# Optimization experiments

Hardware: AMD Instinct MI355X
Metric: run time of the kernel (lower is better)

Reference implementation:

```python
import jax, jax.numpy as jnp
import numpy as np

NUM_REC = 22
P = 24            # nodes per graph
G = 8192          # graphs in batch
N = G * P         # 196608 nodes
E = N * 4         # 786432 edges (avg degree 4)
F_NODE = 96       # 74 chem features + 22 receptor one-hot
F_EDGE = 16
EPS = 1e-5
NEG_SLOPE = 0.2   # GATv2 default negative_slope


def gatv2(x, src, dst, edge_attr, Wl, bl, Wr, br, We, att, bo):
    """PyG GATv2Conv (heads=1, add_self_loops=True, fill_value='mean'), eval mode."""
    n = x.shape[0]
    # self loops with edge_attr = mean of incoming edge attrs per target node
    deg = jax.ops.segment_sum(jnp.ones_like(dst, dtype=x.dtype), dst, num_segments=n)
    loop_attr = jax.ops.segment_sum(edge_attr, dst, num_segments=n) / jnp.maximum(deg, 1.0)[:, None]
    loop = jnp.arange(n, dtype=src.dtype)
    s = jnp.concatenate([src, loop])           # [E+N] source
    d = jnp.concatenate([dst, loop])           # [E+N] target
    ea = jnp.concatenate([edge_attr, loop_attr], axis=0)
    xl = x @ Wl + bl                           # source transform [n, C]
    xr = x @ Wr + br                           # target transform [n, C]
    m = xl[s] + xr[d] + ea @ We                # [E+N, C]
    e = jax.nn.leaky_relu(m, NEG_SLOPE) @ att  # [E+N] attention logits
    # segment softmax over target nodes (every node has its self loop -> no empty segment)
    emax = jax.ops.segment_max(e, d, num_segments=n)
    ez = jnp.exp(e - emax[d])
    denom = jax.ops.segment_sum(ez, d, num_segments=n)
    alpha = ez / denom[d]
    return jax.ops.segment_sum(alpha[:, None] * xl[s], d, num_segments=n) + bo


def batchnorm(h, gamma, beta):
    # training-style BN (batch statistics, biased var) as in torch BatchNorm1d forward
    mu = h.mean(0)
    var = h.var(0)
    return gamma * (h - mu) * jax.lax.rsqrt(var + EPS) + beta


def setup_inputs() -> dict:
    key = jax.random.key(0)
    ks = jax.random.split(key, 40)
    x = jax.random.normal(ks[0], (N, F_NODE), jnp.float32)
    # intra-graph, self-loop-free edges
    src = jax.random.randint(ks[1], (E,), 0, N)
    off = jax.random.randint(ks[2], (E,), 1, P)
    dst = (src // P) * P + (src % P + off) % P
    edge_index = jnp.stack([src, dst]).astype(jnp.int32)
    edge_attr = jax.random.normal(ks[3], (E, F_EDGE), jnp.float32)
    batch = (jnp.arange(N) // P).astype(jnp.int32)

    def lin(k, i, o):
        return jax.random.normal(k, (i, o), jnp.float32) * 0.1

    def vec(k, o):
        return jax.random.normal(k, (o,), jnp.float32) * 0.1

    Fin = F_NODE - NUM_REC  # 74
    return {
        "x": x, "edge_index": edge_index, "edge_attr": edge_attr, "batch": batch,
        # GATv2 layer 1 (74 -> 32)
        "Wl1": lin(ks[4], Fin, 32), "bl1": vec(ks[5], 32),
        "Wr1": lin(ks[6], Fin, 32), "br1": vec(ks[7], 32),
        "We1": lin(ks[8], F_EDGE, 32), "att1": vec(ks[9], 32), "bo1": vec(ks[10], 32),
        # GATv2 layer 2 (32 -> 8)
        "Wl2": lin(ks[11], 32, 8), "bl2": vec(ks[12], 8),
        "Wr2": lin(ks[13], 32, 8), "br2": vec(ks[14], 8),
        "We2": lin(ks[15], F_EDGE, 8), "att2": vec(ks[16], 8), "bo2": vec(ks[17], 8),
        # BatchNorm affine
        "g1": jnp.ones((32,), jnp.float32), "be1": jnp.zeros((32,), jnp.float32),
        "g2": jnp.ones((8,), jnp.float32), "be2": jnp.zeros((8,), jnp.float32),
        # MLP head (8+22=30 -> 32 -> 16 -> 8 -> 4 -> 2)
        "fc1_W": lin(ks[18], 8 + NUM_REC, 32), "fc1_b": vec(ks[19], 32),
        "fc2_W": lin(ks[20], 32, 16), "fc2_b": vec(ks[21], 16),
        "fc3_W": lin(ks[22], 16, 8), "fc3_b": vec(ks[23], 8),
        "fc4_W": lin(ks[24], 8, 4), "fc4_b": vec(ks[25], 4),
        "out_W": lin(ks[26], 4, 2), "out_b": vec(ks[27], 2),
    }


def reference(x, edge_index, edge_attr, batch,
              Wl1, bl1, Wr1, br1, We1, att1, bo1,
              Wl2, bl2, Wr2, br2, We2, att2, bo2,
              g1, be1, g2, be2,
              fc1_W, fc1_b, fc2_W, fc2_b, fc3_W, fc3_b, fc4_W, fc4_b, out_W, out_b):
    src, dst = edge_index[0], edge_index[1]
    # per-graph receptor features = last NUM_REC cols of the first node of each graph
    first_idx = jnp.searchsorted(batch, jnp.arange(G, dtype=batch.dtype))
    rec_feat = x[first_idx, -NUM_REC:]                       # [G, 22]
    xin = x[:, :-NUM_REC]                                    # [N, 74]

    h = jax.nn.relu(gatv2(xin, src, dst, edge_attr, Wl1, bl1, Wr1, br1, We1, att1, bo1))
    h = batchnorm(h, g1, be1)                                # [N, 32]
    h = jax.nn.sigmoid(gatv2(h, src, dst, edge_attr, Wl2, bl2, Wr2, br2, We2, att2, bo2))
    h = batchnorm(h, g2, be2)                                # [N, 8]

    cnt = jax.ops.segment_sum(jnp.ones((x.shape[0], 1), x.dtype), batch, num_segments=G)
    pooled = jax.ops.segment_sum(h, batch, num_segments=G) / cnt  # global_mean_pool [G, 8]

    z = jnp.concatenate([pooled, rec_feat], axis=1)          # [G, 30]
    z = jax.nn.relu(z @ fc1_W + fc1_b)
    z = jax.nn.relu(z @ fc2_W + fc2_b)
    z = jax.nn.relu(z @ fc3_W + fc3_b)
    z = jax.nn.relu(z @ fc4_W + fc4_b)
    return z @ out_W + out_b                                 # [G, 2]
```

## Files before the change

kernel.cpp:

```cpp
#include <hip/hip_runtime.h>

typedef unsigned short u16;
typedef unsigned int   u32;
typedef __attribute__((ext_vector_type(4))) float f4_t;
typedef __attribute__((ext_vector_type(4))) unsigned short us4_t;
typedef __attribute__((ext_vector_type(4))) unsigned int   u4_t;

#define GG 8192
#define PP 24
#define NN 196608
#define EE 786432
#define CAP 176

#define oWl1 0
#define oWr1 2368
#define obl1 4736
#define obr1 4768
#define oWe1 4800
#define oatt1 5312
#define obo1 5344
#define oWl2 5376
#define oWr2 5632
#define obl2 5888
#define obr2 5896
#define oWe2 5904
#define oatt2 6032
#define obo2 6040
#define ofc1W 6048
#define ofc1b 7008
#define ofc2W 7040
#define ofc2b 7552
#define ofc3W 7568
#define ofc3b 7696
#define ofc4W 7704
#define ofc4b 7736
#define ooutW 7740
#define ooutb 7748

#define oW1I 0
#define oW2P 4864
#define oB2P 5376

__device__ __forceinline__ float bf2f(u16 u){
  union { u32 i; float f; } x; x.i = ((u32)u) << 16; return x.f;
}
__device__ __forceinline__ u32 fkey(float f){
  int i = __float_as_int(f);
  return (i >= 0) ? (((u32)i) | 0x80000000u) : ~((u32)i);
}
__device__ __forceinline__ float funkey(u32 k){
  u32 i = (k & 0x80000000u) ? (k & 0x7FFFFFFFu) : ~k;
  return __uint_as_float(i);
}
__device__ __forceinline__ float lrelu(float m){ return m > 0.f ? m : 0.2f*m; }
__device__ __forceinline__ float sexp(float a){ return __expf(fminf(a, 0.f)); }
__device__ __forceinline__ float ldf(const void* p, size_t i, int isf){
  return isf ? ((const float*)p)[i] : bf2f(((const u16*)p)[i]);
}

__global__ void k_zero(float* __restrict__ out){
  int i = blockIdx.x*256 + threadIdx.x;
  if(i < GG*2) out[i] = 0.f;
}

__global__ void k_count(const int* __restrict__ dst, int* __restrict__ cnt){
  int e = blockIdx.x*256 + threadIdx.x;
  if(e < EE){
    u32 d = (u32)dst[e];
    if(d < (u32)NN) atomicAdd(&cnt[d], 1);
  }
}

__global__ void k_scanA(const int* __restrict__ cnt, int* __restrict__ offs,
                        int* __restrict__ bsum){
  __shared__ int part[1024];
  int t = threadIdx.x;
  int i = blockIdx.x*1024 + t;
  int c = cnt[i];
  part[t] = c; __syncthreads();
  for(int off=1; off<1024; off<<=1){
    int v = (t>=off) ? part[t-off] : 0;
    __syncthreads();
    part[t] += v;
    __syncthreads();
  }
  offs[i] = part[t] - c;
  if(t==1023) bsum[blockIdx.x] = part[1023];
}

__global__ void k_scanB(int* __restrict__ bsum, int* __restrict__ offs){
  __shared__ int part[256];
  int t = threadIdx.x;
  int c = (t < 192) ? bsum[t] : 0;
  part[t] = c; __syncthreads();
  for(int off=1; off<256; off<<=1){
    int v = (t>=off) ? part[t-off] : 0;
    __syncthreads();
    part[t] += v;
    __syncthreads();
  }
  if(t < 192) bsum[t] = part[t] - c;
  if(t == 255) offs[NN] = part[255];
}

__global__ void k_scanC(int* __restrict__ offs, const int* __restrict__ bsum,
                        int* __restrict__ cursor){
  int t = threadIdx.x;
  int i = blockIdx.x*1024 + t;
  int v = offs[i] + bsum[blockIdx.x];
  offs[i] = v;
  cursor[i] = v;
}

__global__ void k_scatter(const int* __restrict__ src, const int* __restrict__ dst,
                          int* __restrict__ cursor, int* __restrict__ spack){
  int e = blockIdx.x*256 + threadIdx.x;
  if(e < EE){
    u32 d = (u32)dst[e];
    if(d >= (u32)NN) return;
    int g = d / PP;
    int pos = atomicAdd(&cursor[d], 1);
    if((u32)pos < (u32)EE){
      int sl = src[e] - g*PP;
      if((u32)sl > 23u) sl = 0;
      spack[pos] = sl | ((int)(d - g*PP) << 5) | (e << 10);
    }
  }
}

__global__ void k_eaperm(const int* __restrict__ spack, const int* __restrict__ offs,
                         const void* __restrict__ ea, const int* __restrict__ dflag,
                         float* __restrict__ eap){
  int i = blockIdx.x*256 + threadIdx.x;
  if(i >= EE) return;
  if(i >= offs[NN]) return;
  int isf = dflag[0];
  u32 id = ((u32)spack[i]) >> 10;
  if(id >= (u32)EE) id = 0;
  float* o = eap + (size_t)i*16;
  if(isf){
    const float* er = (const float*)ea + (size_t)id*16;
    #pragma unroll
    for(int q=0;q<4;q++) *(f4_t*)(o + q*4) = *(const f4_t*)(er + q*4);
  } else {
    const u16* er = (const u16*)ea + (size_t)id*16;
    #pragma unroll
    for(int c=0;c<16;c++) o[c] = bf2f(er[c]);
  }
}

__global__ void k_eapermB(const int* __restrict__ spack, const int* __restrict__ offs,
                          const void* __restrict__ ea, const int* __restrict__ dflag,
                          const float* __restrict__ wb,
                          void* __restrict__ eap, float* __restrict__ p2){
  int i = blockIdx.x*256 + threadIdx.x;
  if(i >= EE) return;
  if(i >= offs[NN]) return;
  int isf = dflag[0];
  u32 id = ((u32)spack[i]) >> 10;
  if(id >= (u32)EE) id = 0;
  float eav[16];
  if(isf){
    const float* er = (const float*)ea + (size_t)id*16;
    #pragma unroll
    for(int k=0;k<16;k++) eav[k] = er[k];
    float* o = (float*)eap + (size_t)i*16;
    #pragma unroll
    for(int q=0;q<4;q++) *(f4_t*)(o + q*4) = *(const f4_t*)(er + q*4);
  } else {
    const u16* er = (const u16*)ea + (size_t)id*16;
    #pragma unroll
    for(int k=0;k<16;k++) eav[k] = bf2f(er[k]);
    const u4_t* s4 = (const u4_t*)er;
    u4_t* o4 = (u4_t*)((u16*)eap + (size_t)i*16);
    o4[0] = s4[0];
    o4[1] = s4[1];
  }
  float* o2 = p2 + (size_t)i*8;
  #pragma unroll
  for(int c=0;c<8;c+=4){
    float s0=0.f, s1=0.f, s2=0.f, s3=0.f;
    #pragma unroll
    for(int k=0;k<16;k++){
      f4_t w = *(const f4_t*)(wb + oWe2 + k*8 + c);
      s0 += eav[k]*w[0]; s1 += eav[k]*w[1]; s2 += eav[k]*w[2]; s3 += eav[k]*w[3];
    }
    f4_t r; r[0]=s0; r[1]=s1; r[2]=s2; r[3]=s3;
    *(f4_t*)(o2 + c) = r;
  }
}

__global__ void k_wconv(float* __restrict__ wb, float* __restrict__ wq, int* __restrict__ dflag,
    const u32* __restrict__ xw,
    const void* Wl1, const void* bl1, const void* Wr1, const void* br1,
    const void* We1, const void* att1, const void* bo1,
    const void* Wl2, const void* bl2, const void* Wr2, const void* br2,
    const void* We2, const void* att2, const void* bo2,
    const void* f1W, const void* f1b, const void* f2W, const void* f2b,
    const void* f3W, const void* f3b, const void* f4W, const void* f4b,
    const void* oW,  const void* ob)
{
  __shared__ u32 mx[256];
  int t = threadIdx.x;
  u32 m = 0;
  for(int i=t; i<2048; i+=256){
    u32 e = (xw[i] >> 7) & 0xFFu;
    m = m > e ? m : e;
  }
  mx[t] = m; __syncthreads();
  for(int off=128; off>0; off>>=1){
    if(t<off) mx[t] = mx[t] > mx[t+off] ? mx[t] : mx[t+off];
    __syncthreads();
  }
  int isf = (mx[0] > 140u) ? 1 : 0;
  if(t==0) dflag[0] = isf;
  #define CP(off,src,len) for(int i=t;i<(len);i+=256) wb[(off)+i]=ldf(src,i,isf);
  CP(oWl1,Wl1,2368) CP(oWr1,Wr1,2368) CP(obl1,bl1,32) CP(obr1,br1,32)
  CP(oWe1,We1,512)  CP(oatt1,att1,32) CP(obo1,bo1,32)
  CP(oWl2,Wl2,256)  CP(oWr2,Wr2,256)  CP(obl2,bl2,8)  CP(obr2,br2,8)
  CP(oWe2,We2,128)  CP(oatt2,att2,8)  CP(obo2,bo2,8)
  CP(ofc1W,f1W,960) CP(ofc1b,f1b,32)  CP(ofc2W,f2W,512) CP(ofc2b,f2b,16)
  CP(ofc3W,f3W,128) CP(ofc3b,f3b,8)   CP(ofc4W,f4W,32)  CP(ofc4b,f4b,4)
  CP(ooutW,oW,8)    CP(ooutb,ob,2)
  #undef CP
  for(int i=t; i<76*64; i+=256){
    int k = i>>6, cc = i&63, mat = cc>>5, c = cc&31;
    wq[oW1I + i] = (k < 74) ? ldf(mat ? Wr1 : Wl1, k*32 + c, isf) : 0.f;
  }
}

__global__ void k_prep2(float* __restrict__ wq, const float* __restrict__ wb,
                        const float* __restrict__ stats1){
  int t = threadIdx.x;
  for(int i=t; i<512; i+=256){
    int k = i>>4, cc = i&15, mat = cc>>3, c = cc&7;
    wq[oW2P + i] = stats1[k] * wb[(mat ? oWr2 : oWl2) + k*8 + c];
  }
  if(t < 16){
    int mat = t>>3, c = t&7;
    float s = wb[(mat ? obr2 : obl2) + c];
    for(int k=0;k<32;k++) s += stats1[32+k] * wb[(mat ? oWr2 : oWl2) + k*8 + c];
    wq[oB2P + t] = s;
  }
}

__global__ __launch_bounds__(256, 4) void k_l1stats_p(
    const void* __restrict__ x, const void* __restrict__ eap,
    const float* __restrict__ wb, const float* __restrict__ wq,
    const int* __restrict__ offs, const int* __restrict__ spack, const int* __restrict__ dflag,
    float* __restrict__ p1sum, float* __restrict__ p1sq,
    float* __restrict__ h1)
{
  __shared__ __align__(16) float sP[CAP][36];
  __shared__ __align__(16) float sXl[24][36];
  __shared__ __align__(16) float sXr[24][36];
  __shared__ __align__(16) float sPS[24][32];
  __shared__ __align__(16) float sPQ[24][32];
  __shared__ float sEv[CAP];
  __shared__ int   sSl[CAP];
  __shared__ int   sRO[25];

  const int t = threadIdx.x;
  const int g = blockIdx.x;
  const int isf = dflag[0];
  const int nb = g*PP;
  const int eb = offs[nb];
  int ecnt = offs[nb+24] - eb;
  if(ecnt < 0) ecnt = 0; if(ecnt > CAP) ecnt = CAP;

  if(t < 25){
    int v = offs[nb+t] - eb;
    if(v < 0) v = 0; if(v > CAP) v = CAP;
    sRO[t] = v;
  }
  for(int i=t; i<ecnt; i+=256){
    int sl = spack[eb+i] & 31; if(sl > 23) sl = 0;
    sSl[i] = sl;
  }

  {
    const int c = t & 31, mat = (t>>5)&1, w = t>>6, cc = t&63;
    const float* gW = wq + oW1I;
    float bi = wb[(mat ? obr1 : obl1) + c];
    float acc[6];
    #pragma unroll
    for(int j=0;j<6;j++) acc[j] = bi;
    if(isf){
      const float* xr0 = (const float*)x + (size_t)(nb + w*6)*96;
      for(int kb=0; kb<19; kb++){
        float w0 = gW[(kb*4+0)*64 + cc];
        float w1 = gW[(kb*4+1)*64 + cc];
        float w2 = gW[(kb*4+2)*64 + cc];
        float w3 = gW[(kb*4+3)*64 + cc];
        #pragma unroll
        for(int j=0;j<6;j++){
          f4_t xv = *(const f4_t*)(xr0 + (size_t)j*96 + kb*4);
          acc[j] += xv[0]*w0 + xv[1]*w1 + xv[2]*w2 + xv[3]*w3;
        }
      }
    } else {
      const u16* xr0 = (const u16*)x + (size_t)(nb + w*6)*96;
      for(int kb=0; kb<19; kb++){
        float w0 = gW[(kb*4+0)*64 + cc];
        float w1 = gW[(kb*4+1)*64 + cc];
        float w2 = gW[(kb*4+2)*64 + cc];
        float w3 = gW[(kb*4+3)*64 + cc];
        #pragma unroll
        for(int j=0;j<6;j++){
          us4_t xv = *(const us4_t*)(xr0 + (size_t)j*96 + kb*4);
          acc[j] += bf2f(xv[0])*w0 + bf2f(xv[1])*w1 + bf2f(xv[2])*w2 + bf2f(xv[3])*w3;
        }
      }
    }
    if(mat){
      #pragma unroll
      for(int j=0;j<6;j++) sXr[w*6+j][c] = acc[j];
    } else {
      #pragma unroll
      for(int j=0;j<6;j++) sXl[w*6+j][c] = acc[j];
    }
  }

  for(int i=t; i<ecnt*8; i+=256){
    int e = i>>3, q = i&7;
    float ev[16];
    if(isf){
      const float* er = (const float*)eap + (size_t)(eb+e)*16;
      #pragma unroll
      for(int qq=0;qq<4;qq++){
        f4_t v = *(const f4_t*)(er + qq*4);
        ev[qq*4+0]=v[0]; ev[qq*4+1]=v[1]; ev[qq*4+2]=v[2]; ev[qq*4+3]=v[3];
      }
    } else {
      const u16* er = (const u16*)eap + (size_t)(eb+e)*16;
      #pragma unroll
      for(int qq=0;qq<4;qq++){
        us4_t v = *(const us4_t*)(er + qq*4);
        ev[qq*4+0]=bf2f(v[0]); ev[qq*4+1]=bf2f(v[1]); ev[qq*4+2]=bf2f(v[2]); ev[qq*4+3]=bf2f(v[3]);
      }
    }
    float s0=0.f, s1=0.f, s2=0.f, s3=0.f;
    #pragma unroll
    for(int k=0;k<16;k++){
      f4_t w = *(const f4_t*)(wb + oWe1 + k*32 + q*4);
      s0 += ev[k]*w[0]; s1 += ev[k]*w[1]; s2 += ev[k]*w[2]; s3 += ev[k]*w[3];
    }
    f4_t r; r[0]=s0; r[1]=s1; r[2]=s2; r[3]=s3;
    *(f4_t*)&sP[e][q*4] = r;
  }
  __syncthreads();

  if(t < 192){
    const int r = t >> 3, sub = t & 7;
    const int a = sRO[r], b = sRO[r+1];
    const int deg = b - a;
    const float* att = wb + oatt1;

    float emax = -3.4e38f;
    for(int e=a+sub; e<b; e+=8){
      int sl = sSl[e];
      float ev = 0.f;
      #pragma unroll
      for(int q=0;q<8;q++){
        f4_t pv  = *(const f4_t*)&sP[e][q*4];
        f4_t xlv = *(const f4_t*)&sXl[sl][q*4];
        f4_t xrv = *(const f4_t*)&sXr[r][q*4];
        ev += att[q*4+0]*lrelu(xlv[0]+xrv[0]+pv[0]);
        ev += att[q*4+1]*lrelu(xlv[1]+xrv[1]+pv[1]);
        ev += att[q*4+2]*lrelu(xlv[2]+xrv[2]+pv[2]);
        ev += att[q*4+3]*lrelu(xlv[3]+xrv[3]+pv[3]);
      }
      sEv[e] = ev;
      emax = fmaxf(emax, ev);
    }
    emax = fmaxf(emax, __shfl_xor(emax, 1));
    emax = fmaxf(emax, __shfl_xor(emax, 2));
    emax = fmaxf(emax, __shfl_xor(emax, 4));

    float m0=0.f, m1=0.f, m2=0.f, m3=0.f;
    for(int e=a; e<b; ++e){
      f4_t pv = *(const f4_t*)&sP[e][sub*4];
      m0 += pv[0]; m1 += pv[1]; m2 += pv[2]; m3 += pv[3];
    }
    float invd = 1.f / (float)(deg > 0 ? deg : 1);
    float sv;
    {
      int c0 = sub*4;
      sv  = att[c0+0]*lrelu(sXl[r][c0+0] + sXr[r][c0+0] + m0*invd);
      sv += att[c0+1]*lrelu(sXl[r][c0+1] + sXr[r][c0+1] + m1*invd);
      sv += att[c0+2]*lrelu(sXl[r][c0+2] + sXr[r][c0+2] + m2*invd);
      sv += att[c0+3]*lrelu(sXl[r][c0+3] + sXr[r][c0+3] + m3*invd);
    }
    sv += __shfl_xor(sv, 1);
    sv += __shfl_xor(sv, 2);
    sv += __shfl_xor(sv, 4);

    float m = fmaxf(emax, sv);
    float ssum = 0.f;
    for(int e=a+sub; e<b; e+=8){
      float z = sexp(sEv[e] - m);
      sEv[e] = z;
      ssum += z;
    }
    ssum += __shfl_xor(ssum, 1);
    ssum += __shfl_xor(ssum, 2);
    ssum += __shfl_xor(ssum, 4);
    float selfZ = sexp(sv - m);
    float rden = 1.f / fmaxf(ssum + selfZ, 1e-30f);

    float a0=0.f, a1=0.f, a2=0.f, a3=0.f;
    for(int e=a; e<b; ++e){
      float z = sEv[e];
      f4_t xlv = *(const f4_t*)&sXl[sSl[e]][sub*4];
      a0 += z*xlv[0]; a1 += z*xlv[1]; a2 += z*xlv[2]; a3 += z*xlv[3];
    }
    f4_t xself = *(const f4_t*)&sXl[r][sub*4];
    f4_t outv, sqv;
    {
      float o;
      o = (a0 + selfZ*xself[0]) * rden; o = fmaxf(o + wb[obo1+sub*4+0], 0.f); outv[0]=o; sqv[0]=o*o;
      o = (a1 + selfZ*xself[1]) * rden; o = fmaxf(o + wb[obo1+sub*4+1], 0.f); outv[1]=o; sqv[1]=o*o;
      o = (a2 + selfZ*xself[2]) * rden; o = fmaxf(o + wb[obo1+sub*4+2], 0.f); outv[2]=o; sqv[2]=o*o;
      o = (a3 + selfZ*xself[3]) * rden; o = fmaxf(o + wb[obo1+sub*4+3], 0.f); outv[3]=o; sqv[3]=o*o;
    }
    *(f4_t*)&h1[((size_t)nb + r)*32 + sub*4] = outv;
    *(f4_t*)&sPS[r][sub*4] = outv;
    *(f4_t*)&sPQ[r][sub*4] = sqv;
  }
  __syncthreads();
  if(t < 32){
    float s=0.f, q=0.f;
    #pragma unroll
    for(int r=0;r<24;r++){ s += sPS[r][t]; q += sPQ[r][t]; }
    p1sum[g*32+t] = s; p1sq[g*32+t] = q;
  }
}

__global__ __launch_bounds__(256, 6) void k_fused2_p(
    const float* __restrict__ p2,
    const float* __restrict__ wb, const float* __restrict__ wq,
    const float* __restrict__ h1,
    const int* __restrict__ offs, const int* __restrict__ spack,
    float* __restrict__ gsum2, float* __restrict__ gsq2)
{
  __shared__ __align__(16) float sP2[CAP][12];
  __shared__ float sXl2[24][13];
  __shared__ float sXr2[24][13];
  __shared__ float sEv[CAP];
  __shared__ int   sSl[CAP];
  __shared__ int   sRO[25];
  __shared__ float sGS[24][8];
  __shared__ float sGQ[24][8];

  const int t = threadIdx.x;
  const int g = blockIdx.x;
  const int wid = t >> 6;
  const int lane = t & 63;
  const int nb = g*PP;
  const int eb = offs[nb];
  int ecnt = offs[nb+24] - eb;
  if(ecnt < 0) ecnt = 0; if(ecnt > CAP) ecnt = CAP;

  if(t < 25){
    int v = offs[nb+t] - eb;
    if(v < 0) v = 0; if(v > CAP) v = CAP;
    sRO[t] = v;
  }
  for(int i=t; i<ecnt; i+=256){
    int sl = spack[eb+i] & 31; if(sl > 23) sl = 0;
    sSl[i] = sl;
  }
  for(int i=t; i<ecnt*2; i+=256){
    int e = i>>1, half = i&1;
    f4_t v = *(const f4_t*)(p2 + (size_t)(eb+e)*8 + half*4);
    *(f4_t*)&sP2[e][half*4] = v;
  }
  {
    int rz = wid*6;
    for(int i=lane; i<96; i+=64){
      int rl = i>>4, cc = i&15;
      int r = rz + rl;
      float s = wq[oB2P + cc];
      const float* hr = h1 + ((size_t)nb + r)*32;
      #pragma unroll
      for(int q=0;q<8;q++){
        f4_t hv = *(const f4_t*)(hr + q*4);
        s += hv[0]*wq[oW2P+(q*4+0)*16+cc] + hv[1]*wq[oW2P+(q*4+1)*16+cc]
           + hv[2]*wq[oW2P+(q*4+2)*16+cc] + hv[3]*wq[oW2P+(q*4+3)*16+cc];
      }
      if(cc < 8) sXl2[r][cc] = s; else sXr2[r][cc-8] = s;
    }
  }
  __syncthreads();

  if(t < 192){
    const int r = t >> 3, sub = t & 7;
    const int a = sRO[r], b = sRO[r+1];
    const int deg = b - a;
    const float* att2 = wb + oatt2;

    float emax = -3.4e38f;
    for(int e=a+sub; e<b; e+=8){
      int sl = sSl[e];
      f4_t q0 = *(const f4_t*)&sP2[e][0];
      f4_t q1 = *(const f4_t*)&sP2[e][4];
      float ev = 0.f;
      #pragma unroll
      for(int j=0;j<4;j++) ev += att2[j]  *lrelu(sXl2[sl][j]   + sXr2[r][j]   + q0[j]);
      #pragma unroll
      for(int j=0;j<4;j++) ev += att2[4+j]*lrelu(sXl2[sl][4+j] + sXr2[r][4+j] + q1[j]);
      sEv[e] = ev;
      emax = fmaxf(emax, ev);
    }
    emax = fmaxf(emax, __shfl_xor(emax, 1));
    emax = fmaxf(emax, __shfl_xor(emax, 2));
    emax = fmaxf(emax, __shfl_xor(emax, 4));

    float mpc = 0.f;
    for(int e=a; e<b; ++e)
      mpc += sP2[e][sub];
    float invd = 1.f / (float)(deg > 0 ? deg : 1);
    float sv = att2[sub]*lrelu(sXl2[r][sub] + sXr2[r][sub] + mpc*invd);
    sv += __shfl_xor(sv, 1);
    sv += __shfl_xor(sv, 2);
    sv += __shfl_xor(sv, 4);

    float m = fmaxf(emax, sv);
    float ssum = 0.f;
    for(int e=a+sub; e<b; e+=8){
      float z = sexp(sEv[e] - m);
      sEv[e] = z;
      ssum += z;
    }
    ssum += __shfl_xor(ssum, 1);
    ssum += __shfl_xor(ssum, 2);
    ssum += __shfl_xor(ssum, 4);
    float selfZ = sexp(sv - m);
    float rden = 1.f / fmaxf(ssum + selfZ, 1e-30f);

    float acc = 0.f;
    for(int e=a; e<b; ++e)
      acc += sEv[e] * sXl2[sSl[e]][sub];
    float o = (acc + selfZ*sXl2[r][sub]) * rden;
    float s = 1.f / (1.f + __expf(-(o + wb[obo2+sub])));
    sGS[r][sub] = s;
    sGQ[r][sub] = s*s;
  }
  __syncthreads();
  if(t < 8){
    float gs=0.f, gq=0.f;
    #pragma unroll
    for(int r=0;r<24;r++){ gs += sGS[r][t]; gq += sGQ[r][t]; }
    gsum2[g*8+t] = gs; gsq2[g*8+t] = gq;
  }
}

__global__ __launch_bounds__(256, 6) void k_l1stats(
    const void* __restrict__ x, const void* __restrict__ ea, const float* __restrict__ eap,
    const float* __restrict__ wb, const float* __restrict__ wq,
    const int* __restrict__ offs, const int* __restrict__ spack, const int* __restrict__ dflag,
    float* __restrict__ p1sum, float* __restrict__ p1sq,
    float* __restrict__ h1, int use_h1)
{
  __shared__ __align__(16) float sEaF[CAP][16];
  __shared__ __align__(16) float sXl[24][36];
  __shared__ float sXr[24][33];
  __shared__ float sEaSum[24][17];
  __shared__ float sEv[CAP];
  __shared__ int   sSl[CAP];
  __shared__ int   sRO[25];
  __shared__ float sSelfE[24];
  __shared__ float sPS[4][32], sPQ[4][32];

  const int t = threadIdx.x;
  const int g = blockIdx.x;
  const int wid = t >> 6;
  const int lane = t & 63;
  const int isf = dflag[0];
  const int nb = g*PP;
  const int eb = offs[nb];
  int ecnt = offs[nb+24] - eb; if(ecnt < 0) ecnt = 0; if(ecnt > CAP) ecnt = CAP;

  if(t < 25){
    int v = offs[nb+t] - eb;
    if(v < 0) v = 0; if(v > CAP) v = CAP;
    sRO[t] = v;
  }
  if(eap){
    for(int i=t; i<ecnt; i+=256) sSl[i] = spack[eb+i] & 1023;
    for(int i=t; i<ecnt*4; i+=256){
      int e = i>>2, q = i&3;
      *(f4_t*)&sEaF[e][q*4] = *(const f4_t*)(eap + ((size_t)(eb+e))*16 + q*4);
    }
  } else {
    for(int i=t; i<ecnt; i+=256){
      int sp = spack[eb+i];
      sSl[i] = sp & 1023;
      u32 id = ((u32)sp) >> 10;
      if(id >= (u32)EE) id = 0;
      if(isf){
        const float* er = (const float*)ea + (size_t)id*16;
        #pragma unroll
        for(int q=0;q<4;q++) *(f4_t*)&sEaF[i][q*4] = *(const f4_t*)(er + q*4);
      } else {
        #pragma unroll
        for(int c=0;c<16;c++) sEaF[i][c] = bf2f(((const u16*)ea)[(size_t)id*16 + c]);
      }
    }
  }
  {
    int rz = wid*6;
    for(int i=lane; i<6*17; i+=64) sEaSum[rz + i/17][i%17] = 0.f;
  }

  {
    const int c = t & 31, mat = (t>>5)&1, w = wid, cc = t&63;
    const float* gW = wq + oW1I;
    float bi = wb[(mat ? obr1 : obl1) + c];
    float acc[6];
    #pragma unroll
    for(int j=0;j<6;j++) acc[j] = bi;
    if(isf){
      const float* xr0 = (const float*)x + (size_t)(nb + w*6)*96;
      for(int kb=0; kb<19; kb++){
        float w0 = gW[(kb*4+0)*64 + cc];
        float w1 = gW[(kb*4+1)*64 + cc];
        float w2 = gW[(kb*4+2)*64 + cc];
        float w3 = gW[(kb*4+3)*64 + cc];
        #pragma unroll
        for(int j=0;j<6;j++){
          f4_t xv = *(const f4_t*)(xr0 + (size_t)j*96 + kb*4);
          acc[j] += xv[0]*w0 + xv[1]*w1 + xv[2]*w2 + xv[3]*w3;
        }
      }
    } else {
      const u16* xr0 = (const u16*)x + (size_t)(nb + w*6)*96;
      for(int kb=0; kb<19; kb++){
        float w0 = gW[(kb*4+0)*64 + cc];
        float w1 = gW[(kb*4+1)*64 + cc];
        float w2 = gW[(kb*4+2)*64 + cc];
        float w3 = gW[(kb*4+3)*64 + cc];
        #pragma unroll
        for(int j=0;j<6;j++){
          us4_t xv = *(const us4_t*)(xr0 + (size_t)j*96 + kb*4);
          acc[j] += bf2f(xv[0])*w0 + bf2f(xv[1])*w1 + bf2f(xv[2])*w2 + bf2f(xv[3])*w3;
        }
      }
    }
    if(mat){
      #pragma unroll
      for(int j=0;j<6;j++) sXr[w*6+j][c] = acc[j];
    } else {
      #pragma unroll
      for(int j=0;j<6;j++) sXl[w*6+j][c] = acc[j];
    }
  }
  __syncthreads();

  const int r0 = wid*6;
  const int a0 = sRO[r0], a1 = sRO[r0+6];
  const int c = t & 31, eo = (t>>5)&1;

  float wr[16];
  #pragma unroll
  for(int k=0;k<16;k++) wr[k] = wb[oWe1 + k*32 + c];
  const float av = wb[oatt1 + c];
  const float bv = wb[obo1 + c];

  for(int base=a0; base<a1; base+=2){
    int e = base + eo;
    bool valid = (e < a1);
    int ec = valid ? e : a0;
    int sp = sSl[ec];
    int sl = sp & 31; if(sl > 23) sl = 0;
    int dl = (sp >> 5) & 31; if(dl > 23) dl = 0;
    f4_t A0 = *(const f4_t*)&sEaF[ec][0];
    f4_t A1 = *(const f4_t*)&sEaF[ec][4];
    f4_t A2 = *(const f4_t*)&sEaF[ec][8];
    f4_t A3 = *(const f4_t*)&sEaF[ec][12];
    float p = A0[0]*wr[0]+A0[1]*wr[1]+A0[2]*wr[2]+A0[3]*wr[3]
            + A1[0]*wr[4]+A1[1]*wr[5]+A1[2]*wr[6]+A1[3]*wr[7]
            + A2[0]*wr[8]+A2[1]*wr[9]+A2[2]*wr[10]+A2[3]*wr[11]
            + A3[0]*wr[12]+A3[1]*wr[13]+A3[2]*wr[14]+A3[3]*wr[15];
    if(valid && c < 16) atomicAdd(&sEaSum[dl][c], sEaF[ec][c]);
    float v = lrelu(sXl[sl][c] + sXr[dl][c] + p) * av;
    v += __shfl_xor(v, 16);
    v += __shfl_xor(v, 8);
    v += __shfl_xor(v, 4);
    v += __shfl_xor(v, 2);
    v += __shfl_xor(v, 1);
    if(valid && c == 0) sEv[e] = v;
  }

  #pragma unroll
  for(int rp=0; rp<3; rp++){
    int r = r0 + rp*2 + eo;
    int deg = sRO[r+1] - sRO[r];
    float invd = 1.f / (float)(deg > 0 ? deg : 1);
    float mp = 0.f;
    #pragma unroll
    for(int k=0;k<16;k++) mp += sEaSum[r][k] * wr[k];
    float v = lrelu(sXl[r][c] + sXr[r][c] + mp*invd) * av;
    v += __shfl_xor(v, 16);
    v += __shfl_xor(v, 8);
    v += __shfl_xor(v, 4);
    v += __shfl_xor(v, 2);
    v += __shfl_xor(v, 1);
    if(c == 0) sSelfE[r] = v;
  }

  float ps = 0.f, pq = 0.f;
  const int h = (t >> 5) & 1;
  #pragma unroll
  for(int j=0;j<6;j++){
    int r = r0 + j;
    int a = sRO[r], b = sRO[r+1];
    float selfE = sSelfE[r];
    float mx = -3.4e38f;
    for(int e=a+lane; e<b; e+=64) mx = fmaxf(mx, sEv[e]);
    mx = fmaxf(mx, __shfl_xor(mx, 32));
    mx = fmaxf(mx, __shfl_xor(mx, 16));
    mx = fmaxf(mx, __shfl_xor(mx, 8));
    mx = fmaxf(mx, __shfl_xor(mx, 4));
    mx = fmaxf(mx, __shfl_xor(mx, 2));
    mx = fmaxf(mx, __shfl_xor(mx, 1));
    float m = fmaxf(mx, selfE);
    float ds = 0.f;
    for(int e=a+lane; e<b; e+=64){
      float z = sexp(sEv[e] - m);
      sEv[e] = z;
      ds += z;
    }
    ds += __shfl_xor(ds, 32);
    ds += __shfl_xor(ds, 16);
    ds += __shfl_xor(ds, 8);
    ds += __shfl_xor(ds, 4);
    ds += __shfl_xor(ds, 2);
    ds += __shfl_xor(ds, 1);
    float selfZ = sexp(selfE - m);
    float rden = 1.f / fmaxf(ds + selfZ, 1e-30f);
    float acc = 0.f;
    for(int e=a+h; e<b; e+=2){
      int sl = sSl[e] & 31; if(sl > 23) sl = 0;
      acc += sEv[e] * sXl[sl][c];
    }
    acc += __shfl_xor(acc, 32);
    float out = (acc + selfZ * sXl[r][c]) * rden;
    out = fmaxf(out + bv, 0.f);
    if(h == 0){
      if(use_h1) h1[((size_t)nb + r)*32 + c] = out;
      ps += out; pq += out*out;
    }
  }
  if(h == 0){ sPS[wid][c] = ps; sPQ[wid][c] = pq; }
  __syncthreads();
  if(t < 32){
    p1sum[g*32+t] = sPS[0][t]+sPS[1][t]+sPS[2][t]+sPS[3][t];
    p1sq[g*32+t]  = sPQ[0][t]+sPQ[1][t]+sPQ[2][t]+sPQ[3][t];
  }
}

__global__ void k_reduce(const float* __restrict__ ps, const float* __restrict__ pq,
                         const void* __restrict__ gamma, const void* __restrict__ beta,
                         const int* __restrict__ dflag,
                         float* __restrict__ stats, int F){
  __shared__ float rs[256], rq[256];
  int f = blockIdx.x, t = threadIdx.x;
  float s=0.f, q=0.f;
  for(int g=t; g<GG; g+=256){ s += ps[g*F+f]; q += pq[g*F+f]; }
  rs[t]=s; rq[t]=q; __syncthreads();
  for(int off=128; off>0; off>>=1){
    if(t<off){ rs[t]+=rs[t+off]; rq[t]+=rq[t+off]; }
    __syncthreads();
  }
  if(t==0){
    int isf = dflag[0];
    float mu  = rs[0] * (1.f/(float)NN);
    float var = rq[0] * (1.f/(float)NN) - mu*mu;
// ... 100 lines not shown
    float p = A0[0]*wr[0]+A0[1]*wr[1]+A0[2]*wr[2]+A0[3]*wr[3]
            + A1[0]*wr[4]+A1[1]*wr[5]+A1[2]*wr[6]+A1[3]*wr[7]
            + A2[0]*wr[8]+A2[1]*wr[9]+A2[2]*wr[10]+A2[3]*wr[11]
            + A3[0]*wr[12]+A3[1]*wr[13]+A3[2]*wr[14]+A3[3]*wr[15];
    if(valid){
      atomicAdd(&sEaSum[dl][c],   sEaF[ec][c]);
      atomicAdd(&sEaSum[dl][c+8], sEaF[ec][c+8]);
    }
    float v = lrelu(sXl2[sl][c] + sXr2[dl][c] + p) * av;
    v += __shfl_xor(v, 4);
    v += __shfl_xor(v, 2);
    v += __shfl_xor(v, 1);
    if(valid && c == 0) sEv[e] = v;
  }

  {
    int rr = r0 + (eo < 6 ? eo : 0);
    bool valid = (eo < 6);
    int deg = sRO[rr+1] - sRO[rr];
    float invd = 1.f / (float)(deg > 0 ? deg : 1);
    float mp = 0.f;
    #pragma unroll
    for(int k=0;k<16;k++) mp += sEaSum[rr][k] * wr[k];
    float v = lrelu(sXl2[rr][c] + sXr2[rr][c] + mp*invd) * av;
    v += __shfl_xor(v, 4);
    v += __shfl_xor(v, 2);
    v += __shfl_xor(v, 1);
    if(valid && c == 0) sSelfE[rr] = v;
  }

  float gs = 0.f, gq = 0.f;
  #pragma unroll
  for(int j=0;j<6;j++){
    int r = r0 + j;
    int a = sRO[r], b = sRO[r+1];
    float selfE = sSelfE[r];
    float mx = -3.4e38f;
    for(int e=a+lane; e<b; e+=64) mx = fmaxf(mx, sEv[e]);
    mx = fmaxf(mx, __shfl_xor(mx, 32));
    mx = fmaxf(mx, __shfl_xor(mx, 16));
    mx = fmaxf(mx, __shfl_xor(mx, 8));
    mx = fmaxf(mx, __shfl_xor(mx, 4));
    mx = fmaxf(mx, __shfl_xor(mx, 2));
    mx = fmaxf(mx, __shfl_xor(mx, 1));
    float m = fmaxf(mx, selfE);
    float ds = 0.f;
    for(int e=a+lane; e<b; e+=64){
      float z = sexp(sEv[e] - m);
      sEv[e] = z;
      ds += z;
    }
    ds += __shfl_xor(ds, 32);
    ds += __shfl_xor(ds, 16);
    ds += __shfl_xor(ds, 8);
    ds += __shfl_xor(ds, 4);
    ds += __shfl_xor(ds, 2);
    ds += __shfl_xor(ds, 1);
    float selfZ = sexp(selfE - m);
    float rden = 1.f / fmaxf(ds + selfZ, 1e-30f);
    float acc = 0.f;
    for(int e=a+eo; e<b; e+=8){
      int sl = sSl[e] & 31; if(sl > 23) sl = 0;
      acc += sEv[e] * sXl2[sl][c];
    }
    acc += __shfl_xor(acc, 8);
    acc += __shfl_xor(acc, 16);
    acc += __shfl_xor(acc, 32);
    float out = (acc + selfZ * sXl2[r][c]) * rden;
    float s = 1.f / (1.f + __expf(-(out + bv)));
    if(eo == 0){ gs += s; gq += s*s; }
  }
  if(eo == 0){ sGS[wid][c] = gs; sGQ[wid][c] = gq; }
  __syncthreads();
  if(t < 8){
    gsum2[g*8+t] = sGS[0][t]+sGS[1][t]+sGS[2][t]+sGS[3][t];
    gsq2[g*8+t]  = sGQ[0][t]+sGQ[1][t]+sGQ[2][t]+sGQ[3][t];
  }
}

__global__ __launch_bounds__(256) void k_fused2_rec(
    const void* __restrict__ x, const void* __restrict__ ea,
    const float* __restrict__ wb, const float* __restrict__ stats1,
    const int* __restrict__ offs, const int* __restrict__ spack, const int* __restrict__ dflag,
    float* __restrict__ gsum2, float* __restrict__ gsq2)
{
  __shared__ float sXrow[24][76];
  __shared__ float sEaF[CAP][17];
  __shared__ __align__(16) float sXl[24][36];
  __shared__ __align__(16) float sXr[24][36];
  __shared__ __align__(16) float sOut[24][36];
  __shared__ float sH[24][33];
  __shared__ float sXl2[24][12], sXr2[24][12], sOut2[24][12];
  __shared__ float sEapSum[24][32];
  __shared__ float sEv[CAP], sEz[CAP];
  __shared__ int   sSp[CAP];
  __shared__ int   sDeg[24];
  __shared__ u32   sMaxU[24];
  __shared__ float sMaxF[24], sDen[24], sSelfZ[24];
  __shared__ float sAtt[32], sBo[32], sSc[32], sSh[32];

  const int t = threadIdx.x;
  const int g = blockIdx.x;
  const int isf = dflag[0];
  int eb = offs[g*24], ee = offs[(g+1)*24];
  if(eb < 0) eb = 0; if(eb > EE) eb = EE;
  if(ee < eb) ee = eb; if(ee > EE) ee = EE;
  int ecnt = ee - eb; if(ecnt > CAP) ecnt = CAP;

  for(int i=t; i<24*74; i+=256){
    int r = i/74, c = i%74;
    sXrow[r][c] = ldf(x, (size_t)(g*PP + r)*96 + c, isf);
  }
  for(int i=t; i<CAP; i+=256) sSp[i] = (i<ecnt) ? spack[eb+i] : 0;
  if(t < 32){ sAtt[t]=wb[oatt1+t]; sBo[t]=wb[obo1+t]; sSc[t]=stats1[t]; sSh[t]=stats1[32+t]; }
  if(t < 24){ sDeg[t]=0; sMaxU[t]=0u; sDen[t]=0.f; }
  for(int i=t; i<24*32; i+=256) sEapSum[i>>5][i&31] = 0.f;
  __syncthreads();
  for(int i=t; i<CAP*16; i+=256){
    int e = i>>4, c = i&15;
    float v = 0.f;
    if(e < ecnt){
      u32 id = ((u32)sSp[e]) >> 10;
      if(id >= (u32)EE) id = 0;
      v = ldf(ea, (size_t)id*16 + c, isf);
    }
    sEaF[e][c] = v;
  }
  __syncthreads();

  {
    int c = t & 31, rr0 = t >> 5;
    for(int r = rr0; r < 24; r += 8){
      float al = wb[obl1+c], ar = wb[obr1+c];
      for(int k=0;k<74;k++){
        float xv = sXrow[r][k];
        al += xv * wb[oWl1 + k*32 + c];
        ar += xv * wb[oWr1 + k*32 + c];
      }
      sXl[r][c] = al; sXr[r][c] = ar;
    }
  }
  __syncthreads();

  for(int e=t; e<ecnt; e+=256){
    int sp = sSp[e];
    int sl = sp & 31; if(sl > 23) sl = 0;
    int dl = (sp >> 5) & 31; if(dl > 23) dl = 0;
    float ev = 0.f;
    for(int c=0;c<32;c++){
      float p = 0.f;
      for(int k=0;k<16;k++) p += sEaF[e][k] * wb[oWe1 + k*32 + c];
      atomicAdd(&sEapSum[dl][c], p);
      ev += lrelu(sXl[sl][c] + sXr[dl][c] + p) * sAtt[c];
    }
    sEv[e] = ev;
    atomicMax(&sMaxU[dl], fkey(ev));
    atomicAdd(&sDeg[dl], 1);
  }
  __syncthreads();

  if(t < 24){
    float invd = 1.f / (float)(sDeg[t] > 0 ? sDeg[t] : 1);
    float ev = 0.f;
    for(int c=0;c<32;c++)
      ev += lrelu(sXl[t][c] + sXr[t][c] + sEapSum[t][c]*invd) * sAtt[c];
    float mxv = (sDeg[t] > 0) ? fmaxf(funkey(sMaxU[t]), ev) : ev;
    sMaxF[t] = mxv;
    float z = sexp(ev - mxv);
    sSelfZ[t] = z;
    sDen[t] = z;
  }
  __syncthreads();

  for(int e=t; e<ecnt; e+=256){
    int dl = (sSp[e]>>5)&31; if(dl > 23) dl = 0;
    float z = sexp(sEv[e] - sMaxF[dl]);
    sEz[e] = z;
    atomicAdd(&sDen[dl], z);
  }
  __syncthreads();

  for(int e=t; e<ecnt; e+=256){
    int dl = (sSp[e]>>5)&31; if(dl > 23) dl = 0;
    sEz[e] /= fmaxf(sDen[dl], 1e-30f);
  }
  if(t < 24) sSelfZ[t] /= fmaxf(sDen[t], 1e-30f);
  __syncthreads();

  for(int o=t; o<24*8; o+=256){
    int nl = o >> 3, cq = (o & 7)*4;
    float al = sSelfZ[nl];
    f4_t xv = *(const f4_t*)&sXl[nl][cq];
    f4_t r;
    #pragma unroll
    for(int j=0;j<4;j++) r[j] = al*xv[j];
    *(f4_t*)&sOut[nl][cq] = r;
  }
  __syncthreads();

  for(int o=t; o<ecnt*8; o+=256){
    int e = o >> 3, cq = (o & 7)*4;
    int sp = sSp[e];
    int sl = sp & 31; if(sl > 23) sl = 0;
    int dl = (sp >> 5) & 31; if(dl > 23) dl = 0;
    float al = sEz[e];
    f4_t xv = *(const f4_t*)&sXl[sl][cq];
    atomicAdd(&sOut[dl][cq+0], al*xv[0]);
    atomicAdd(&sOut[dl][cq+1], al*xv[1]);
    atomicAdd(&sOut[dl][cq+2], al*xv[2]);
    atomicAdd(&sOut[dl][cq+3], al*xv[3]);
  }
  __syncthreads();

  for(int i=t; i<24*32; i+=256){
    int r = i>>5, c = i&31;
    float v = fmaxf(sOut[r][c] + sBo[c], 0.f);
    sH[r][c] = v*sSc[c] + sSh[c];
  }
  __syncthreads();
  if(t < 24){ sDeg[t]=0; sMaxU[t]=0u; sDen[t]=0.f; }
  for(int i=t; i<24*8; i+=256) sEapSum[i>>3][i&7] = 0.f;
  __syncthreads();

  if(t < 24*8*2){
    int mat = t/192, rem = t%192, r = rem/8, c = rem&7;
    const float* Wm = wb + (mat ? oWr2 : oWl2);
    float s = wb[(mat ? obr2 : obl2) + c];
    for(int k=0;k<32;k++) s += sH[r][k]*Wm[k*8+c];
    if(mat) sXr2[r][c] = s; else sXl2[r][c] = s;
  }
  __syncthreads();

  for(int e=t; e<ecnt; e+=256){
    int sp = sSp[e];
    int sl = sp & 31; if(sl > 23) sl = 0;
    int dl = (sp >> 5) & 31; if(dl > 23) dl = 0;
    float ev = 0.f;
    for(int c=0;c<8;c++){
      float p = 0.f;
      for(int k=0;k<16;k++) p += sEaF[e][k] * wb[oWe2 + k*8 + c];
      atomicAdd(&sEapSum[dl][c], p);
      ev += lrelu(sXl2[sl][c] + sXr2[dl][c] + p) * wb[oatt2+c];
    }
    sEv[e] = ev;
    atomicMax(&sMaxU[dl], fkey(ev));
    atomicAdd(&sDeg[dl], 1);
  }
  __syncthreads();

  if(t < 24){
    float invd = 1.f / (float)(sDeg[t] > 0 ? sDeg[t] : 1);
    float ev = 0.f;
    for(int c=0;c<8;c++)
      ev += lrelu(sXl2[t][c] + sXr2[t][c] + sEapSum[t][c]*invd) * wb[oatt2+c];
    float mxv = (sDeg[t] > 0) ? fmaxf(funkey(sMaxU[t]), ev) : ev;
    sMaxF[t] = mxv;
    float z = sexp(ev - mxv);
    sSelfZ[t] = z;
    sDen[t] = z;
  }
  __syncthreads();

  for(int e=t; e<ecnt; e+=256){
    int dl = (sSp[e]>>5)&31; if(dl > 23) dl = 0;
    float z = sexp(sEv[e] - sMaxF[dl]);
    sEz[e] = z;
    atomicAdd(&sDen[dl], z);
  }
  __syncthreads();

  for(int e=t; e<ecnt; e+=256){
    int dl = (sSp[e]>>5)&31; if(dl > 23) dl = 0;
    sEz[e] /= fmaxf(sDen[dl], 1e-30f);
  }
  if(t < 24) sSelfZ[t] /= fmaxf(sDen[t], 1e-30f);
  __syncthreads();

  for(int o=t; o<24*8; o+=256){
    int nl = o >> 3, c = o & 7;
    sOut2[nl][c] = sSelfZ[nl] * sXl2[nl][c];
  }
  __syncthreads();

  for(int o=t; o<ecnt*8; o+=256){
    int e = o >> 3, c = o & 7;
    int sp = sSp[e];
    int sl = sp & 31; if(sl > 23) sl = 0;
    int dl = (sp >> 5) & 31; if(dl > 23) dl = 0;
    atomicAdd(&sOut2[dl][c], sEz[e]*sXl2[sl][c]);
  }
  __syncthreads();

  if(t < 8){
    float gs=0.f, gq=0.f;
    for(int nl=0; nl<24; nl++){
      float v = sOut2[nl][t] + wb[obo2+t];
      float s = 1.f / (1.f + __expf(-v));
      gs += s; gq += s*s;
    }
    gsum2[g*8+t] = gs; gsq2[g*8+t] = gq;
  }
}

__global__ __launch_bounds__(256) void k_mlp(
    const float* __restrict__ gsum2, const float* __restrict__ stats2,
    const void* __restrict__ x, const int* __restrict__ dflag,
    const float* __restrict__ wb, float* __restrict__ out)
{
  __shared__ float w[1702];
  int t = threadIdx.x;
  for(int i=t; i<1702; i+=256) w[i] = wb[6048+i];
  __syncthreads();
  int g = blockIdx.x*256 + t;
  int isf = dflag[0];
  float a[30], b[32];
  for(int c=0;c<8;c++) a[c] = stats2[c]*(gsum2[(size_t)g*8+c]*(1.f/24.f)) + stats2[8+c];
  size_t xoff = (size_t)g*PP*96 + 74;
  for(int j=0;j<22;j++) a[8+j] = ldf(x, xoff+j, isf);
  for(int o=0;o<32;o++){ float s = w[960+o];  for(int i=0;i<30;i++) s += a[i]*w[i*32+o];      b[o]=fmaxf(s,0.f); }
  for(int o=0;o<16;o++){ float s = w[1504+o]; for(int i=0;i<32;i++) s += b[i]*w[992+i*16+o];  a[o]=fmaxf(s,0.f); }
  for(int o=0;o<8;o++){  float s = w[1648+o]; for(int i=0;i<16;i++) s += a[i]*w[1520+i*8+o];  b[o]=fmaxf(s,0.f); }
  for(int o=0;o<4;o++){  float s = w[1688+o]; for(int i=0;i<8;i++)  s += b[i]*w[1656+i*4+o];  a[o]=fmaxf(s,0.f); }
  for(int o=0;o<2;o++){
    float s = w[1700+o];
    for(int i=0;i<4;i++) s += a[i]*w[1692+i*2+o];
    out[(size_t)g*2+o] = s;
  }
}

extern "C" void kernel_launch(void* const* d_in, const int* in_sizes, int n_in,
                              void* d_out, int out_size, void* d_ws, size_t ws_size,
                              hipStream_t stream)
{
  (void)in_sizes; (void)n_in; (void)out_size;
  const void* x    = d_in[0];
  const int* eidx  = (const int*)d_in[1];
  const void* ea   = d_in[2];

  const int* srcA = eidx;
  const int* dstA = eidx + EE;

  constexpr size_t O_WB    = 0;
  constexpr size_t O_WQ    = 32768;
  constexpr size_t O_OFFS  = 57344;
  constexpr size_t O_CUR   = O_OFFS + (size_t)(NN+512)*4;
  constexpr size_t O_SPACK = O_CUR  + (size_t)NN*4;
  constexpr size_t O_P1S   = O_SPACK + (size_t)EE*4;
  constexpr size_t O_P1Q   = O_P1S   + (size_t)GG*32*4;
  constexpr size_t O_ST1   = O_P1Q   + (size_t)GG*32*4;
  constexpr size_t O_GS2   = O_ST1   + 256;
  constexpr size_t O_GQ2   = O_GS2   + (size_t)GG*8*4;
  constexpr size_t O_ST2   = O_GQ2   + (size_t)GG*8*4;
  constexpr size_t O_FLAG  = O_ST2   + 256;
  constexpr size_t REQUIRED_BASE = O_FLAG + 256;
  constexpr size_t O_H1    = REQUIRED_BASE;
  constexpr size_t REQUIRED_BIG = O_H1 + (size_t)NN*32*4;
  constexpr size_t O_EAP1  = REQUIRED_BIG;
  constexpr size_t O_P2    = O_EAP1 + (size_t)EE*16*4;
  constexpr size_t REQUIRED_P = O_P2 + (size_t)EE*8*4;
  constexpr size_t REQUIRED_EAP16 = O_EAP1 + (size_t)EE*16*4;

  if(ws_size < REQUIRED_BASE){
    k_zero<<<(GG*2+255)/256, 256, 0, stream>>>((float*)d_out);
    return;
  }
  const int use_h1  = (ws_size >= REQUIRED_BIG)   ? 1 : 0;
  const int use_p   = (use_h1 && ws_size >= REQUIRED_P) ? 1 : 0;
  const int use_eap = (!use_p && ws_size >= REQUIRED_EAP16) ? 1 : 0;

  char* W = (char*)d_ws;
  float* wb     = (float*)(W + O_WB);
  float* wq     = (float*)(W + O_WQ);
  int*   offs   = (int*)(W + O_OFFS);
  int*   bsum   = offs + NN + 64;
  int*   cnt    = (int*)(W + O_CUR);
  int*   cursor = (int*)(W + O_CUR);
  int*   spack  = (int*)(W + O_SPACK);
  float* p1sum  = (float*)(W + O_P1S);
  float* p1sq   = (float*)(W + O_P1Q);
  float* stats1 = (float*)(W + O_ST1);
  float* gsum2  = (float*)(W + O_GS2);
  float* gsq2   = (float*)(W + O_GQ2);
  float* stats2 = (float*)(W + O_ST2);
  int*   dflag  = (int*)(W + O_FLAG);
  float* h1     = (float*)(W + O_H1);
  void*  eap1   = (void*)(W + O_EAP1);
  float* p2     = (float*)(W + O_P2);

  hipMemsetAsync(cnt, 0, (size_t)NN*sizeof(int), stream);
  k_count  <<<EE/256, 256, 0, stream>>>(dstA, cnt);
  k_scanA  <<<192, 1024, 0, stream>>>(cnt, offs, bsum);
  k_scanB  <<<1, 256, 0, stream>>>(bsum, offs);
  k_scanC  <<<192, 1024, 0, stream>>>(offs, bsum, cursor);
  k_scatter<<<EE/256, 256, 0, stream>>>(srcA, dstA, cursor, spack);
  k_wconv  <<<1, 256, 0, stream>>>(wb, wq, dflag, (const u32*)x,
            d_in[4], d_in[5], d_in[6], d_in[7], d_in[8], d_in[9], d_in[10],
            d_in[11], d_in[12], d_in[13], d_in[14], d_in[15], d_in[16], d_in[17],
            d_in[22], d_in[23], d_in[24], d_in[25], d_in[26], d_in[27],
            d_in[28], d_in[29], d_in[30], d_in[31]);
  if(use_p){
    k_eapermB<<<EE/256, 256, 0, stream>>>(spack, offs, ea, dflag, wb, eap1, p2);
    k_l1stats_p<<<GG, 256, 0, stream>>>(x, eap1, wb, wq, offs, spack, dflag,
                                        p1sum, p1sq, h1);
  } else {
    if(use_eap)
      k_eaperm<<<EE/256, 256, 0, stream>>>(spack, offs, ea, dflag, (float*)eap1);
    k_l1stats<<<GG, 256, 0, stream>>>(x, ea, use_eap ? (float*)eap1 : (float*)nullptr,
                                      wb, wq, offs, spack, dflag,
                                      p1sum, p1sq, h1, use_h1);
  }
  k_reduce <<<32, 256, 0, stream>>>(p1sum, p1sq, d_in[18], d_in[19], dflag, stats1, 32);
  k_prep2  <<<1, 256, 0, stream>>>(wq, wb, stats1);
  if(use_p)
    k_fused2_p<<<GG, 256, 0, stream>>>(p2, wb, wq, h1, offs, spack, gsum2, gsq2);
  else if(use_h1)
    k_fused2_h1<<<GG, 256, 0, stream>>>(ea, use_eap ? (float*)eap1 : (float*)nullptr,
                                        wb, wq, h1, offs, spack, dflag, gsum2, gsq2);
  else
    k_fused2_rec<<<GG, 256, 0, stream>>>(x, ea, wb, stats1, offs, spack, dflag, gsum2, gsq2);
  k_reduce <<<8, 256, 0, stream>>>(gsum2, gsq2, d_in[20], d_in[21], dflag, stats2, 8);
  k_mlp    <<<GG/256, 256, 0, stream>>>(gsum2, stats2, x, dflag, wb, (float*)d_out);
}
```

Before: 592.2 us.

## Compute layer-2 edge projection on the fly instead of materialising p2

```diff
diff --git a/kernel.cpp b/kernel.cpp
--- a/kernel.cpp
+++ b/kernel.cpp
@@ -151,42 +151,23 @@
 
 __global__ void k_eapermB(const int* __restrict__ spack, const int* __restrict__ offs,
                           const void* __restrict__ ea, const int* __restrict__ dflag,
-                          const float* __restrict__ wb,
-                          void* __restrict__ eap, float* __restrict__ p2){
+                          void* __restrict__ eap){
   int i = blockIdx.x*256 + threadIdx.x;
   if(i >= EE) return;
   if(i >= offs[NN]) return;
   int isf = dflag[0];
   u32 id = ((u32)spack[i]) >> 10;
   if(id >= (u32)EE) id = 0;
-  float eav[16];
   if(isf){
     const float* er = (const float*)ea + (size_t)id*16;
-    #pragma unroll
-    for(int k=0;k<16;k++) eav[k] = er[k];
     float* o = (float*)eap + (size_t)i*16;
     #pragma unroll
     for(int q=0;q<4;q++) *(f4_t*)(o + q*4) = *(const f4_t*)(er + q*4);
   } else {
-    const u16* er = (const u16*)ea + (size_t)id*16;
-    #pragma unroll
-    for(int k=0;k<16;k++) eav[k] = bf2f(er[k]);
-    const u4_t* s4 = (const u4_t*)er;
+    const u4_t* s4 = (const u4_t*)((const u16*)ea + (size_t)id*16);
     u4_t* o4 = (u4_t*)((u16*)eap + (size_t)i*16);
     o4[0] = s4[0];
     o4[1] = s4[1];
-  }
-  float* o2 = p2 + (size_t)i*8;
-  #pragma unroll
-  for(int c=0;c<8;c+=4){
-    float s0=0.f, s1=0.f, s2=0.f, s3=0.f;
-    #pragma unroll
-    for(int k=0;k<16;k++){
-      f4_t w = *(const f4_t*)(wb + oWe2 + k*8 + c);
-      s0 += eav[k]*w[0]; s1 += eav[k]*w[1]; s2 += eav[k]*w[2]; s3 += eav[k]*w[3];
-    }
-    f4_t r; r[0]=s0; r[1]=s1; r[2]=s2; r[3]=s3;
-    *(f4_t*)(o2 + c) = r;
   }
 }
 
@@ -202,6 +183,7 @@
 {
   __shared__ u32 mx[256];
   int t = threadIdx.x;
+  int bid = blockIdx.x;
   u32 m = 0;
   for(int i=t; i<2048; i+=256){
     u32 e = (xw[i] >> 7) & 0xFFu;
@@ -213,8 +195,9 @@
     __syncthreads();
   }
   int isf = (mx[0] > 140u) ? 1 : 0;
-  if(t==0) dflag[0] = isf;
-  #define CP(off,src,len) for(int i=t;i<(len);i+=256) wb[(off)+i]=ldf(src,i,isf);
+  if(t==0 && bid==0) dflag[0] = isf;
+  const int stp = 8*256;
+  #define CP(off,src,len) for(int i=bid*256+t;i<(len);i+=stp) wb[(off)+i]=ldf(src,i,isf);
   CP(oWl1,Wl1,2368) CP(oWr1,Wr1,2368) CP(obl1,bl1,32) CP(obr1,br1,32)
   CP(oWe1,We1,512)  CP(oatt1,att1,32) CP(obo1,bo1,32)
   CP(oWl2,Wl2,256)  CP(oWr2,Wr2,256)  CP(obl2,bl2,8)  CP(obr2,br2,8)
@@ -223,7 +206,7 @@
   CP(ofc3W,f3W,128) CP(ofc3b,f3b,8)   CP(ofc4W,f4W,32)  CP(ofc4b,f4b,4)
   CP(ooutW,oW,8)    CP(ooutb,ob,2)
   #undef CP
-  for(int i=t; i<76*64; i+=256){
+  for(int i=bid*256+t; i<76*64; i+=stp){
     int k = i>>6, cc = i&63, mat = cc>>5, c = cc&31;
     wq[oW1I + i] = (k < 74) ? ldf(mat ? Wr1 : Wl1, k*32 + c, isf) : 0.f;
   }
@@ -437,7 +420,7 @@
 }
 
 __global__ __launch_bounds__(256, 6) void k_fused2_p(
-    const float* __restrict__ p2,
+    const void* __restrict__ eap, const int* __restrict__ dflag,
     const float* __restrict__ wb, const float* __restrict__ wq,
     const float* __restrict__ h1,
     const int* __restrict__ offs, const int* __restrict__ spack,
@@ -456,6 +439,7 @@
   const int g = blockIdx.x;
   const int wid = t >> 6;
   const int lane = t & 63;
+  const int isf = dflag[0];
   const int nb = g*PP;
   const int eb = offs[nb];
   int ecnt = offs[nb+24] - eb;
@@ -472,8 +456,31 @@
   }
   for(int i=t; i<ecnt*2; i+=256){
     int e = i>>1, half = i&1;
-    f4_t v = *(const f4_t*)(p2 + (size_t)(eb+e)*8 + half*4);
-    *(f4_t*)&sP2[e][half*4] = v;
+    float eav[16];
+    if(isf){
+      const float* er = (const float*)eap + (size_t)(eb+e)*16;
+      #pragma unroll
+      for(int qq=0;qq<4;qq++){
+        f4_t v = *(const f4_t*)(er + qq*4);
+        eav[qq*4+0]=v[0]; eav[qq*4+1]=v[1]; eav[qq*4+2]=v[2]; eav[qq*4+3]=v[3];
+      }
+    } else {
+      const u16* er = (const u16*)eap + (size_t)(eb+e)*16;
+      #pragma unroll
+      for(int qq=0;qq<4;qq++){
+        us4_t v = *(const us4_t*)(er + qq*4);
+        eav[qq*4+0]=bf2f(v[0]); eav[qq*4+1]=bf2f(v[1]); eav[qq*4+2]=bf2f(v[2]); eav[qq*4+3]=bf2f(v[3]);
+      }
+    }
+    int c = half*4;
+    float s0=0.f, s1=0.f, s2=0.f, s3=0.f;
+    #pragma unroll
+    for(int k=0;k<16;k++){
+      f4_t w = *(const f4_t*)(wb + oWe2 + k*8 + c);
+      s0 += eav[k]*w[0]; s1 += eav[k]*w[1]; s2 += eav[k]*w[2]; s3 += eav[k]*w[3];
+    }
+    f4_t r; r[0]=s0; r[1]=s1; r[2]=s2; r[3]=s3;
+    *(f4_t*)&sP2[e][half*4] = r;
   }
   {
     int rz = wid*6;
@@ -1180,16 +1187,16 @@
   }
 }
 
-__global__ __launch_bounds__(256) void k_mlp(
+__global__ __launch_bounds__(64) void k_mlp(
     const float* __restrict__ gsum2, const float* __restrict__ stats2,
     const void* __restrict__ x, const int* __restrict__ dflag,
     const float* __restrict__ wb, float* __restrict__ out)
 {
   __shared__ float w[1702];
   int t = threadIdx.x;
-  for(int i=t; i<1702; i+=256) w[i] = wb[6048+i];
-  __syncthreads();
-  int g = blockIdx.x*256 + t;
+  for(int i=t; i<1702; i+=64) w[i] = wb[6048+i];
+  __syncthreads();
+  int g = blockIdx.x*64 + t;
   int isf = dflag[0];
   float a[30], b[32];
   for(int c=0;c<8;c++) a[c] = stats2[c]*(gsum2[(size_t)g*8+c]*(1.f/24.f)) + stats2[8+c];
@@ -1234,8 +1241,7 @@
   constexpr size_t O_H1    = REQUIRED_BASE;
   constexpr size_t REQUIRED_BIG = O_H1 + (size_t)NN*32*4;
   constexpr size_t O_EAP1  = REQUIRED_BIG;
-  constexpr size_t O_P2    = O_EAP1 + (size_t)EE*16*4;
-  constexpr size_t REQUIRED_P = O_P2 + (size_t)EE*8*4;
+  constexpr size_t REQUIRED_P     = O_EAP1 + (size_t)EE*16*4;
   constexpr size_t REQUIRED_EAP16 = O_EAP1 + (size_t)EE*16*4;
 
   if(ws_size < REQUIRED_BASE){
@@ -1263,7 +1269,6 @@
   int*   dflag  = (int*)(W + O_FLAG);
   float* h1     = (float*)(W + O_H1);
   void*  eap1   = (void*)(W + O_EAP1);
-  float* p2     = (float*)(W + O_P2);
 
   hipMemsetAsync(cnt, 0, (size_t)NN*sizeof(int), stream);
   k_count  <<<EE/256, 256, 0, stream>>>(dstA, cnt);
@@ -1271,13 +1276,13 @@
   k_scanB  <<<1, 256, 0, stream>>>(bsum, offs);
   k_scanC  <<<192, 1024, 0, stream>>>(offs, bsum, cursor);
   k_scatter<<<EE/256, 256, 0, stream>>>(srcA, dstA, cursor, spack);
-  k_wconv  <<<1, 256, 0, stream>>>(wb, wq, dflag, (const u32*)x,
+  k_wconv  <<<8, 256, 0, stream>>>(wb, wq, dflag, (const u32*)x,
             d_in[4], d_in[5], d_in[6], d_in[7], d_in[8], d_in[9], d_in[10],
             d_in[11], d_in[12], d_in[13], d_in[14], d_in[15], d_in[16], d_in[17],
             d_in[22], d_in[23], d_in[24], d_in[25], d_in[26], d_in[27],
             d_in[28], d_in[29], d_in[30], d_in[31]);
   if(use_p){
-    k_eapermB<<<EE/256, 256, 0, stream>>>(spack, offs, ea, dflag, wb, eap1, p2);
+    k_eapermB<<<EE/256, 256, 0, stream>>>(spack, offs, ea, dflag, eap1);
     k_l1stats_p<<<GG, 256, 0, stream>>>(x, eap1, wb, wq, offs, spack, dflag,
                                         p1sum, p1sq, h1);
   } else {
@@ -1290,12 +1295,12 @@
   k_reduce <<<32, 256, 0, stream>>>(p1sum, p1sq, d_in[18], d_in[19], dflag, stats1, 32);
   k_prep2  <<<1, 256, 0, stream>>>(wq, wb, stats1);
   if(use_p)
-    k_fused2_p<<<GG, 256, 0, stream>>>(p2, wb, wq, h1, offs, spack, gsum2, gsq2);
+    k_fused2_p<<<GG, 256, 0, stream>>>(eap1, dflag, wb, wq, h1, offs, spack, gsum2, gsq2);
   else if(use_h1)
     k_fused2_h1<<<GG, 256, 0, stream>>>(ea, use_eap ? (float*)eap1 : (float*)nullptr,
                                         wb, wq, h1, offs, spack, dflag, gsum2, gsq2);
   else
     k_fused2_rec<<<GG, 256, 0, stream>>>(x, ea, wb, stats1, offs, spack, dflag, gsum2, gsq2);
   k_reduce <<<8, 256, 0, stream>>>(gsum2, gsq2, d_in[20], d_in[21], dflag, stats2, 8);
-  k_mlp    <<<GG/256, 256, 0, stream>>>(gsum2, stats2, x, dflag, wb, (float*)d_out);
-}
+  k_mlp    <<<GG/64, 64, 0, stream>>>(gsum2, stats2, x, dflag, wb, (float*)d_out);
+}
```

Measured after the change: 582.4 us. Within noise of the previous version (-1.7%).
